# Kernel tuning notes

Measured on AMD Instinct MI355X. Metric: run time of the kernel, lower is better.

## Reference

```python
import jax, jax.numpy as jnp
import numpy as np

# ---- module hyperparameters (init_kwargs) ----
FRAME_LENGTH = 2048
SAMPLE_RATE = 22050
LAG_MIN = 22
LAG_MAX = 2048  # defaults to frame_length
N_BIN = 20
EPS = 1e-7


def _lag2midi(lag, sr):
    return 12.0 * np.log2(sr / (440.0 * lag)) + 69.0


def _midi2lag(midi, sr):
    return sr / (440.0 * 2.0 ** ((midi - 69.0) / 12.0))


def _make_constants():
    midi_min = int(np.ceil(_lag2midi(LAG_MAX, SAMPLE_RATE)))
    midi_max = int(_lag2midi(LAG_MIN, SAMPLE_RATE))
    midi = np.arange(midi_min, midi_max + 1, 1.0 / N_BIN).astype(np.float32)
    lags = _midi2lag(midi.astype(np.float64), SAMPLE_RATE).astype(np.float32)
    lags_ceil = np.ceil(lags).astype(np.int32)
    lags_floor = np.floor(lags).astype(np.int32)
    return (jnp.asarray(lags), jnp.asarray(lags_ceil), jnp.asarray(lags_floor))


LAGS, LAGS_CEIL, LAGS_FLOOR = _make_constants()
RAMP = jnp.arange(1, LAG_MAX, dtype=jnp.float32)  # [tau_max-1]


def setup_inputs() -> dict:
    key = jax.random.key(0)
    x = jax.random.normal(key, (16, 1024, FRAME_LENGTH), dtype=jnp.float32)
    return {"x": x}


def reference(x) -> jnp.ndarray:
    W = FRAME_LENGTH
    tau = LAG_MAX
    # cumulative energy: s[k] = sum_{n<k} x[n]^2, length W+1 (left-padded)
    pad = [(0, 0)] * (x.ndim - 1) + [(1, 0)]
    x0 = jnp.pad(x, pad)
    s = jnp.cumsum(x0 * x0, axis=-1)  # [..., W+1]
    term1 = jnp.flip(s[..., W - tau + 1:], axis=-1)       # [..., tau]
    term2 = s[..., W:] - s[..., :tau]                      # [..., tau]
    # FFT-based autocorrelation r[k] = sum_n x[n] x[n+k], k in [0, tau)
    nfft = 2 * W  # >= 2W-1, linear (non-circular) autocorrelation
    X = jnp.fft.rfft(x, nfft, axis=-1)
    r = jnp.fft.irfft(X * jnp.conj(X), nfft, axis=-1)[..., :tau]
    # YIN difference function and cumulative-mean normalization
    d = (term1 + term2 - 2.0 * r)[..., 1:]                 # [..., tau-1]
    d = RAMP * d / (jnp.cumsum(d, axis=-1) + EPS)
    d0 = jnp.pad(d, pad, constant_values=1.0)              # [..., tau]
    # linear interpolation at fractional midi-grid lags (gather)
    numer = (LAGS - LAGS_FLOOR) * (d0[..., LAGS_CEIL] - d0[..., LAGS_FLOOR])
    denom = (LAGS_CEIL - LAGS_FLOOR).astype(jnp.float32)
    y = numer / denom + d0[..., LAGS_FLOOR]                # [..., M]
    return y
```

## Files before the change

kernel.cpp:

```cpp
#include <hip/hip_runtime.h>
#include <math.h>

typedef __bf16 bf16_t;
typedef __bf16 bf16x8 __attribute__((ext_vector_type(8)));
typedef float  f32x4  __attribute__((ext_vector_type(4)));
typedef float  f32x16 __attribute__((ext_vector_type(16)));
typedef unsigned int u32;
typedef u32 u32x4 __attribute__((ext_vector_type(4)));

#define FRAME 2048
#define NOUT  1580

#define A_STRIDE 2120
#define P_STRIDE 2304
#define B_OFF_BYTES 36864
#define DBUF_OFF_BYTES 36864
#define SARR_OFF_BYTES 45056
#define WTOT_OFF_BYTES 53264
#define SMEM_BYTES 53280

__global__ __launch_bounds__(256, 3) void yingram_kernel(
    const float* __restrict__ x, float* __restrict__ out,
    const int4* __restrict__ tbl, int use_tbl)
{
    __shared__ alignas(16) char smem[SMEM_BYTES];
    bf16_t* arrA    = (bf16_t*)smem;
    char*   arrBb   = smem + B_OFF_BYTES;
    float*  partial = (float*)smem;
    float*  dbuf    = (float*)(smem + DBUF_OFF_BYTES);
    float*  s_arr   = (float*)(smem + SARR_OFF_BYTES);
    float*  wtot    = (float*)(smem + WTOT_OFF_BYTES);

    const int tid  = threadIdx.x;
    const int lane = tid & 63;
    const int w    = tid >> 6;
    const int q    = lane >> 5;
    const int col  = lane & 31;
    const float* xp = x + (size_t)blockIdx.x * FRAME;

    if (tid < 64) {
        int sel = tid & 7;
        int c = (sel < 3) ? sel : sel + 257;
        u32x4 z = {0u,0u,0u,0u};
        *(u32x4*)(arrA + (tid >> 3) * A_STRIDE + 8 * c) = z;
    } else if (tid < 191) {
        int B = tid + 193;
        u32x4 z = {0u,0u,0u,0u};
        *(u32x4*)(arrBb + 16 * (B + (B >> 3))) = z;
    }

    f32x4 f0 = {0,0,0,0}, f1 = {0,0,0,0}, f2, f3;
    const f32x4* xv4 = (const f32x4*)(xp + 8 * tid - 8);
    if (tid != 0) { f0 = xv4[0]; f1 = xv4[1]; }
    f2 = xv4[2]; f3 = xv4[3];

    float xf[16];
    #pragma unroll
    for (int i = 0; i < 4; ++i) {
        xf[i] = f0[i]; xf[4+i] = f1[i]; xf[8+i] = f2[i]; xf[12+i] = f3[i];
    }
    u32 W[8];
    #pragma unroll
    for (int j = 0; j < 8; ++j) {
        union { bf16_t h[2]; u32 u; } cv;
        cv.h[0] = (bf16_t)xf[2*j];
        cv.h[1] = (bf16_t)xf[2*j+1];
        W[j] = cv.u;
    }

    u32x4 D7;
    #pragma unroll
    for (int p = 0; p < 8; ++p) {
        int a = p >> 1;
        u32x4 D;
        if ((p & 1) == 0) {
            D[0] = W[a]; D[1] = W[a+1]; D[2] = W[a+2]; D[3] = W[a+3];
        } else {
            #pragma unroll
            for (int i = 0; i < 4; ++i)
                D[i] = (W[a+i] >> 16) | (W[a+i+1] << 16);
        }
        *(u32x4*)(arrA + p * A_STRIDE + 8 * (tid + 3)) = D;
        if (p == 7) D7 = D;
    }
    *(u32x4*)(arrBb + 16 * (tid + (tid >> 3))) = D7;

    if (tid == 255) {
        #pragma unroll
        for (int p = 0; p < 8; ++p) {
            int a = p >> 1;
            u32x4 D;
            #pragma unroll
            for (int i = 0; i < 4; ++i) {
                int lo = 4 + a + i;
                if ((p & 1) == 0) {
                    D[i] = (lo <= 7) ? W[lo] : 0u;
                } else {
                    u32 x0 = (lo <= 7) ? (W[lo] >> 16) : 0u;
                    u32 x1 = (lo + 1 <= 7) ? (W[lo+1] << 16) : 0u;
                    D[i] = x0 | x1;
                }
            }
            *(u32x4*)(arrA + p * A_STRIDE + 8 * 259) = D;
        }
        u32x4 Db = { W[7] >> 16, 0u, 0u, 0u };
        *(u32x4*)(arrBb + 16 * (256 + (256 >> 3))) = Db;
    }

    float sq[8], pe[8];
    {
        float run = 0.f;
        #pragma unroll
        for (int e = 0; e < 8; ++e) {
            float v = xf[8 + e];
            sq[e] = v * v; run += sq[e]; pe[e] = run;
        }
    }
    float tsum = pe[7];
    float sc = tsum;
    #pragma unroll
    for (int off = 1; off < 64; off <<= 1) {
        float o = __shfl_up(sc, off, 64);
        if (lane >= off) sc += o;
    }
    if (lane == 63) wtot[w] = sc;
    float thr_off = sc - tsum;

    __syncthreads();

    {
        float b0 = wtot[0], b1 = wtot[1], b2 = wtot[2];
        float base = (w > 0 ? b0 : 0.f) + (w > 1 ? b1 : 0.f) + (w > 2 ? b2 : 0.f) + thr_off;
        f32x4 sA, sB;
        #pragma unroll
        for (int i = 0; i < 4; ++i) {
            sA[i] = base + pe[i]   - sq[i];
            sB[i] = base + pe[4+i] - sq[4+i];
        }
        *(f32x4*)(s_arr + 8 * tid)     = sA;
        *(f32x4*)(s_arr + 8 * tid + 4) = sB;
        if (tid == 255) s_arr[2048] = base + pe[7];
    }

    const bf16_t* aPtr = arrA + (col & 7) * A_STRIDE + (col & ~7) + 8 * q + 16 * w;
    int B0 = 2 * w + q + 4 * col;
    const bf16_t* bPtr = (const bf16_t*)arrBb + 8 * (B0 + (B0 >> 3));
    f32x16 acc0, acc1;
    #pragma unroll
    for (int v = 0; v < 16; ++v) { acc0[v] = 0.f; acc1[v] = 0.f; }

    bf16x8 fifo[16];
    #pragma unroll
    for (int i = 0; i < 16; ++i) {
        bf16x8 av = *(const bf16x8*)aPtr;
        bf16x8 bv = *(const bf16x8*)bPtr;
        acc0 = __builtin_amdgcn_mfma_f32_32x32x16_bf16(av, bv, acc0, 0, 0, 0);
        fifo[i] = av;
        aPtr += 64; bPtr += 72;
    }
    #pragma unroll
    for (int i = 0; i < 16; ++i) {
        bf16x8 av = *(const bf16x8*)aPtr;
        bf16x8 bv = *(const bf16x8*)bPtr;
        acc0 = __builtin_amdgcn_mfma_f32_32x32x16_bf16(av, bv, acc0, 0, 0, 0);
        acc1 = __builtin_amdgcn_mfma_f32_32x32x16_bf16(fifo[i], bv, acc1, 0, 0, 0);
        fifo[i] = av;
        aPtr += 64; bPtr += 72;
    }
    if (w < 2) {
        bf16x8 av = *(const bf16x8*)aPtr;
        bf16x8 bv = *(const bf16x8*)bPtr;
        acc0 = __builtin_amdgcn_mfma_f32_32x32x16_bf16(av, bv, acc0, 0, 0, 0);
        if (w == 0)
            acc1 = __builtin_amdgcn_mfma_f32_32x32x16_bf16(fifo[0], bv, acc1, 0, 0, 0);
    }

    __syncthreads();

    float* prow = partial + w * P_STRIDE;
    #pragma unroll
    for (int g = 0; g < 4; ++g) {
        int L0 = 28 + 32 * col - 8 * g - 4 * q;
        int i0 = L0 + 4 * (L0 >> 5);
        f32x4 v0 = { acc0[4*g+3], acc0[4*g+2], acc0[4*g+1], acc0[4*g] };
        *(f32x4*)(prow + i0) = v0;
        int L1 = L0 + 1024;
        int i1 = L1 + 4 * (L1 >> 5);
        f32x4 v1 = { acc1[4*g+3], acc1[4*g+2], acc1[4*g+1], acc1[4*g] };
        *(f32x4*)(prow + i1) = v1;
    }
    __syncthreads();

    const int tb = 8 * tid;
    const int ip = tb + 4 * (tb >> 5);
    f32x4 rA = {0,0,0,0}, rB = {0,0,0,0};
    #pragma unroll
    for (int ww = 0; ww < 4; ++ww) {
        rA += *(f32x4*)(partial + ww * P_STRIDE + ip);
        rB += *(f32x4*)(partial + ww * P_STRIDE + ip + 4);
    }
    const float sW = s_arr[2048];
    f32x4 s0v = *(f32x4*)(s_arr + tb);
    f32x4 s1v = *(f32x4*)(s_arr + tb + 4);
    f32x4 q0  = *(f32x4*)(s_arr + 2040 - tb);
    f32x4 q1  = *(f32x4*)(s_arr + 2044 - tb);
    float e0  = s_arr[2048 - tb];

    float dr[8], pe2[8];
    {
        float term1[8] = { e0, q1[3], q1[2], q1[1], q1[0], q0[3], q0[2], q0[1] };
        float rr[8] = { rA[0],rA[1],rA[2],rA[3], rB[0],rB[1],rB[2],rB[3] };
        float ss[8] = { s0v[0],s0v[1],s0v[2],s0v[3], s1v[0],s1v[1],s1v[2],s1v[3] };
        #pragma unroll
        for (int e = 0; e < 8; ++e)
            dr[e] = term1[e] + sW - ss[e] - 2.f * rr[e];
        if (tid == 0) dr[0] = 0.f;
        float run = 0.f;
        #pragma unroll
        for (int e = 0; e < 8; ++e) { run += dr[e]; pe2[e] = run; }
    }
    float tsum2 = pe2[7];
    float sc2 = tsum2;
    #pragma unroll
    for (int off = 1; off < 64; off <<= 1) {
        float o = __shfl_up(sc2, off, 64);
        if (lane >= off) sc2 += o;
    }
    if (lane == 63) wtot[w] = sc2;
    float thr2 = sc2 - tsum2;
    __syncthreads();

    {
        float b0 = wtot[0], b1 = wtot[1], b2 = wtot[2];
        float base = (w > 0 ? b0 : 0.f) + (w > 1 ? b1 : 0.f) + (w > 2 ? b2 : 0.f) + thr2;
        f32x4 dA, dB;
        #pragma unroll
        for (int i = 0; i < 4; ++i) {
            float cumA = base + pe2[i];
            float cumB = base + pe2[4+i];
            dA[i] = (float)(tb + i)     * dr[i]   / (cumA + 1e-7f);
            dB[i] = (float)(tb + 4 + i) * dr[4+i] / (cumB + 1e-7f);
        }
        *(f32x4*)(dbuf + tb)     = dA;
        *(f32x4*)(dbuf + tb + 4) = dB;
    }
    __syncthreads();

    float* op = out + (size_t)blockIdx.x * NOUT;
    if (use_tbl) {
        for (int m = tid; m < NOUT; m += 256) {
            int4 e = tbl[m];
            float wd = __int_as_float(e.z);
            float df = dbuf[e.x], dc = dbuf[e.y];
            op[m] = wd * (dc - df) + df;
        }
    } else {
        for (int m = tid; m < NOUT; m += 256) {
            double midi = 5.0 + (double)m * 0.05;
            float  mf   = (float)midi;
            double lag64 = 22050.0 / (440.0 * exp2(((double)mf - 69.0) / 12.0));
            float  lag  = (float)lag64;
            float  cf = ceilf(lag), ff = floorf(lag);
            float  dc = dbuf[(int)cf], df = dbuf[(int)ff];
            op[m] = (lag - ff) * (dc - df) / (cf - ff) + df;
        }
    }
}

__global__ void table_kernel(int4* __restrict__ tbl) {
    int m = blockIdx.x * 256 + threadIdx.x;
    if (m >= NOUT) return;
    double midi = 5.0 + (double)m * 0.05;
    float  mf   = (float)midi;
    double lag64 = 22050.0 / (440.0 * exp2(((double)mf - 69.0) / 12.0));
    float  lag  = (float)lag64;
    float  cf = ceilf(lag), ff = floorf(lag);
    float  wd = (cf > ff) ? (lag - ff) / (cf - ff) : 0.f;
    int4 e; e.x = (int)ff; e.y = (int)cf; e.z = __float_as_int(wd); e.w = 0;
    tbl[m] = e;
}

extern "C" void kernel_launch(void* const* d_in, const int* in_sizes, int n_in,
                              void* d_out, int out_size, void* d_ws, size_t ws_size,
                              hipStream_t stream) {
    const float* x = (const float*)d_in[0];
    float* out = (float*)d_out;
    int frames = in_sizes[0] / FRAME;
    int use_tbl = (ws_size >= (size_t)NOUT * sizeof(int4)) ? 1 : 0;
    int4* tbl = (int4*)d_ws;
    if (use_tbl)
        table_kernel<<<dim3((NOUT + 255) / 256), dim3(256), 0, stream>>>(tbl);
    yingram_kernel<<<dim3(frames), dim3(256), 0, stream>>>(x, out, tbl, use_tbl);
}
```

Measured before the change: 313.8 us.

## Shrink shared memory via XOR swizzle and buffer aliasing to fit four blocks

After: 309.5 us. No clear change (-1.4%).

```diff
diff --git a/kernel.cpp b/kernel.cpp
--- a/kernel.cpp
+++ b/kernel.cpp
@@ -12,24 +12,24 @@
 #define NOUT  1580
 
 #define A_STRIDE 2120
-#define P_STRIDE 2304
-#define B_OFF_BYTES 36864
-#define DBUF_OFF_BYTES 36864
-#define SARR_OFF_BYTES 45056
-#define WTOT_OFF_BYTES 53264
-#define SMEM_BYTES 53280
-
-__global__ __launch_bounds__(256, 3) void yingram_kernel(
+#define PROW 2048
+#define B_OFF_BYTES 33920
+#define SARR_OFF_BYTES 32768
+#define SMEM_BYTES 40960
+
+__device__ __forceinline__ int swz(int u) { return u ^ ((u >> 3) & 7); }
+
+__global__ __launch_bounds__(256, 4) void yingram_kernel(
     const float* __restrict__ x, float* __restrict__ out,
     const int4* __restrict__ tbl, int use_tbl)
 {
     __shared__ alignas(16) char smem[SMEM_BYTES];
     bf16_t* arrA    = (bf16_t*)smem;
     char*   arrBb   = smem + B_OFF_BYTES;
+    float*  wtot1   = (float*)(smem + B_OFF_BYTES + 128);
     float*  partial = (float*)smem;
-    float*  dbuf    = (float*)(smem + DBUF_OFF_BYTES);
     float*  s_arr   = (float*)(smem + SARR_OFF_BYTES);
-    float*  wtot    = (float*)(smem + WTOT_OFF_BYTES);
+    float*  dbuf    = (float*)smem;
 
     const int tid  = threadIdx.x;
     const int lane = tid & 63;
@@ -123,23 +123,22 @@
         float o = __shfl_up(sc, off, 64);
         if (lane >= off) sc += o;
     }
-    if (lane == 63) wtot[w] = sc;
+    if (lane == 63) wtot1[w] = sc;
     float thr_off = sc - tsum;
 
     __syncthreads();
 
-    {
-        float b0 = wtot[0], b1 = wtot[1], b2 = wtot[2];
+    f32x4 sA, sB;
+    float sW;
+    {
+        float b0 = wtot1[0], b1 = wtot1[1], b2 = wtot1[2], b3 = wtot1[3];
         float base = (w > 0 ? b0 : 0.f) + (w > 1 ? b1 : 0.f) + (w > 2 ? b2 : 0.f) + thr_off;
-        f32x4 sA, sB;
+        sW = b0 + b1 + b2 + b3;
         #pragma unroll
         for (int i = 0; i < 4; ++i) {
             sA[i] = base + pe[i]   - sq[i];
             sB[i] = base + pe[4+i] - sq[4+i];
         }
-        *(f32x4*)(s_arr + 8 * tid)     = sA;
-        *(f32x4*)(s_arr + 8 * tid + 4) = sB;
-        if (tid == 255) s_arr[2048] = base + pe[7];
     }
 
     const bf16_t* aPtr = arrA + (col & 7) * A_STRIDE + (col & ~7) + 8 * q + 16 * w;
@@ -177,40 +176,39 @@
 
     __syncthreads();
 
-    float* prow = partial + w * P_STRIDE;
+    float* prow = partial + w * PROW;
     #pragma unroll
     for (int g = 0; g < 4; ++g) {
         int L0 = 28 + 32 * col - 8 * g - 4 * q;
-        int i0 = L0 + 4 * (L0 >> 5);
         f32x4 v0 = { acc0[4*g+3], acc0[4*g+2], acc0[4*g+1], acc0[4*g] };
-        *(f32x4*)(prow + i0) = v0;
+        *(f32x4*)(prow + (swz(L0 >> 2) << 2)) = v0;
         int L1 = L0 + 1024;
-        int i1 = L1 + 4 * (L1 >> 5);
         f32x4 v1 = { acc1[4*g+3], acc1[4*g+2], acc1[4*g+1], acc1[4*g] };
-        *(f32x4*)(prow + i1) = v1;
-    }
+        *(f32x4*)(prow + (swz(L1 >> 2) << 2)) = v1;
+    }
+    *(f32x4*)(s_arr + (swz(2 * tid) << 2))     = sA;
+    *(f32x4*)(s_arr + (swz(2 * tid + 1) << 2)) = sB;
     __syncthreads();
 
     const int tb = 8 * tid;
-    const int ip = tb + 4 * (tb >> 5);
+    const int o0 = swz(2 * tid) << 2;
+    const int o1 = swz(2 * tid + 1) << 2;
     f32x4 rA = {0,0,0,0}, rB = {0,0,0,0};
     #pragma unroll
     for (int ww = 0; ww < 4; ++ww) {
-        rA += *(f32x4*)(partial + ww * P_STRIDE + ip);
-        rB += *(f32x4*)(partial + ww * P_STRIDE + ip + 4);
-    }
-    const float sW = s_arr[2048];
-    f32x4 s0v = *(f32x4*)(s_arr + tb);
-    f32x4 s1v = *(f32x4*)(s_arr + tb + 4);
-    f32x4 q0  = *(f32x4*)(s_arr + 2040 - tb);
-    f32x4 q1  = *(f32x4*)(s_arr + 2044 - tb);
-    float e0  = s_arr[2048 - tb];
+        rA += *(f32x4*)(partial + ww * PROW + o0);
+        rB += *(f32x4*)(partial + ww * PROW + o1);
+    }
+    const int uq0 = 510 - 2 * tid;
+    f32x4 q0  = *(f32x4*)(s_arr + (swz(uq0) << 2));
+    f32x4 q1  = *(f32x4*)(s_arr + (swz(uq0 + 1) << 2));
+    float e0  = s_arr[swz((uq0 + 2) & 511) << 2];
 
     float dr[8], pe2[8];
     {
         float term1[8] = { e0, q1[3], q1[2], q1[1], q1[0], q0[3], q0[2], q0[1] };
         float rr[8] = { rA[0],rA[1],rA[2],rA[3], rB[0],rB[1],rB[2],rB[3] };
-        float ss[8] = { s0v[0],s0v[1],s0v[2],s0v[3], s1v[0],s1v[1],s1v[2],s1v[3] };
+        float ss[8] = { sA[0],sA[1],sA[2],sA[3], sB[0],sB[1],sB[2],sB[3] };
         #pragma unroll
         for (int e = 0; e < 8; ++e)
             dr[e] = term1[e] + sW - ss[e] - 2.f * rr[e];
@@ -226,13 +224,15 @@
         float o = __shfl_up(sc2, off, 64);
         if (lane >= off) sc2 += o;
     }
-    if (lane == 63) wtot[w] = sc2;
+    if (lane == 63) partial[PROW + (swz(128 * w + 126) << 2)] = sc2;
     float thr2 = sc2 - tsum2;
     __syncthreads();
 
     {
-        float b0 = wtot[0], b1 = wtot[1], b2 = wtot[2];
-        float base = (w > 0 ? b0 : 0.f) + (w > 1 ? b1 : 0.f) + (w > 2 ? b2 : 0.f) + thr2;
+        float c0 = partial[PROW + (swz(126) << 2)];
+        float c1 = partial[PROW + (swz(254) << 2)];
+        float c2 = partial[PROW + (swz(382) << 2)];
+        float base = (w > 0 ? c0 : 0.f) + (w > 1 ? c1 : 0.f) + (w > 2 ? c2 : 0.f) + thr2;
         f32x4 dA, dB;
         #pragma unroll
         for (int i = 0; i < 4; ++i) {
```
